# Performance work log

Hardware: AMD Instinct MI355X
Metric: run time of the kernel (lower is better)

The kernel has to match this reference:

```python
import jax, jax.numpy as jnp
import numpy as np

N_NODES = 100000
N_EDGES = 1600000
D_FEAT = 128


def sage_conv(x, src, dst, Wl, Wr, b, n_nodes):
    # gather source features, mean-aggregate at destination (PyG SAGEConv, aggr='mean')
    msgs = x[src]                                            # [E, d]
    agg_sum = jax.ops.segment_sum(msgs, dst, num_segments=n_nodes)
    cnt = jax.ops.segment_sum(jnp.ones((src.shape[0],), dtype=x.dtype), dst,
                              num_segments=n_nodes)
    mean = agg_sum / jnp.maximum(cnt, 1.0)[:, None]
    return mean @ Wl + x @ Wr + b


def setup_inputs() -> dict:
    key = jax.random.key(0)
    ks = jax.random.split(key, 9)
    def w(k, shape):
        fan_in = shape[0]
        return jax.random.normal(k, shape, dtype=jnp.float32) / np.sqrt(fan_in)
    x = jax.random.normal(ks[0], (N_NODES, D_FEAT), dtype=jnp.float32)
    edge_index = jax.random.randint(ks[1], (2, N_EDGES), 0, N_NODES, dtype=jnp.int64)
    return {
        "x": x,
        "edge_index": edge_index,
        "W1l": w(ks[2], (D_FEAT, 64)), "W1r": w(ks[3], (D_FEAT, 64)), "b1": jnp.zeros((64,), jnp.float32),
        "W2l": w(ks[4], (64, 128)),    "W2r": w(ks[5], (64, 128)),    "b2": jnp.zeros((128,), jnp.float32),
        "W3l": w(ks[6], (128, 64)),    "W3r": w(ks[7], (128, 64)),    "b3": jnp.zeros((64,), jnp.float32),
        "Wlin": w(ks[8], (64, 10)),    "blin": jnp.zeros((10,), jnp.float32),
    }


def reference(x, edge_index, W1l, W1r, b1, W2l, W2r, b2, W3l, W3r, b3, Wlin, blin):
    n = x.shape[0]
    src, dst = edge_index[0], edge_index[1]
    # dropout omitted (evaluated in inference / identity form)
    h = jnp.tanh(sage_conv(x, src, dst, W1l, W1r, b1, n))
    h = jnp.tanh(sage_conv(h, src, dst, W2l, W2r, b2, n))
    h = jnp.tanh(sage_conv(h, src, dst, W3l, W3r, b3, n))
    return h @ Wlin + blin
```

## Files before the change

kernel.cpp:

```cpp
#include <hip/hip_runtime.h>

#define THREADS 256
#define NB 256
#define NB_SHIFT 8
#define TILE_E 4096
#define EPT 16
#define BMAXPAD 512
#define WT_LD 136

typedef unsigned short ushort_t;
typedef __attribute__((ext_vector_type(8))) short bf16x8;
typedef __attribute__((ext_vector_type(4))) float f32x4;

__device__ __forceinline__ unsigned short f2bf(float f) {
    unsigned u = __float_as_uint(f);
    u += 0x7fff + ((u >> 16) & 1);
    return (unsigned short)(u >> 16);
}
__device__ __forceinline__ float bf2f(unsigned short s) {
    return __uint_as_float((unsigned)s << 16);
}
__device__ __forceinline__ float4 bf4_to_f4(ushort4 u) {
    return make_float4(bf2f(u.x), bf2f(u.y), bf2f(u.z), bf2f(u.w));
}
__device__ __forceinline__ ushort4 f4_to_bf4(float4 v) {
    ushort4 o;
    o.x = f2bf(v.x); o.y = f2bf(v.y); o.z = f2bf(v.z); o.w = f2bf(v.w);
    return o;
}
__device__ __forceinline__ unsigned pack_bf2(float a, float b) {
    return (unsigned)f2bf(a) | ((unsigned)f2bf(b) << 16);
}
__device__ __forceinline__ void acc_pair(unsigned u, float& lo, float& hi) {
    lo += __uint_as_float(u << 16);
    hi += __uint_as_float(u);
}

__global__ __launch_bounds__(64)
void detect_kernel(const unsigned* __restrict__ ei_words, int* __restrict__ flag) {
    if (threadIdx.x == 0 && blockIdx.x == 0) {
        int allzero = 1;
        for (int i = 0; i < 64; ++i) {
            if (ei_words[2 * i + 1] != 0u) { allzero = 0; break; }
        }
        *flag = allzero;
    }
}

__device__ __forceinline__ void load_edge(const void* ei, int is64, int E, int i,
                                          int& s, int& t) {
    if (is64) {
        const long long* p = (const long long*)ei;
        s = (int)p[i];
        t = (int)p[E + i];
    } else {
        const int* p = (const int*)ei;
        s = p[i];
        t = p[E + i];
    }
}

__global__ __launch_bounds__(256)
void tilesort_kernel(const void* __restrict__ ei, const int* __restrict__ flag,
                     unsigned* __restrict__ tbuf, int* __restrict__ tcnt,
                     int* __restrict__ tstart, int E, int B) {
    __shared__ int hist[BMAXPAD];
    __shared__ int wsum[8];
    const int t   = blockIdx.x;
    const int e0  = t * TILE_E;
    const int is64 = *flag;
    unsigned w[EPT];
    unsigned short bk[EPT];
    for (int i = threadIdx.x; i < BMAXPAD; i += 256) hist[i] = 0;
    __syncthreads();
#pragma unroll
    for (int k = 0; k < EPT; ++k) {
        const int i = e0 + k * 256 + (int)threadIdx.x;
        bk[k] = 0xFFFFu;
        w[k]  = 0u;
        if (i < E) {
            int s, d;
            load_edge(ei, is64, E, i, s, d);
            w[k]  = (unsigned)s | ((unsigned)(d & (NB - 1)) << 17);
            bk[k] = (unsigned short)(d >> NB_SHIFT);
            atomicAdd(&hist[bk[k]], 1);
        }
    }
    __syncthreads();
    const int lane = threadIdx.x & 63;
    const int wid  = threadIdx.x >> 6;
    const int v0 = hist[2 * threadIdx.x];
    const int v1 = hist[2 * threadIdx.x + 1];
    const int sum = v0 + v1;
    int incl = sum;
#pragma unroll
    for (int off = 1; off < 64; off <<= 1) {
        int tt = __shfl_up(incl, off, 64);
        if (lane >= off) incl += tt;
    }
    if (lane == 63) wsum[wid] = incl;
    __syncthreads();
    int woff = 0;
    for (int ww = 0; ww < wid; ++ww) woff += wsum[ww];
    const int excl = woff + incl - sum;
    hist[2 * threadIdx.x]     = excl;
    hist[2 * threadIdx.x + 1] = excl + v0;
    const int b0 = 2 * threadIdx.x, b1 = 2 * threadIdx.x + 1;
    if (b0 < B) { tcnt[(size_t)t * B + b0] = v0; tstart[(size_t)t * B + b0] = excl; }
    if (b1 < B) { tcnt[(size_t)t * B + b1] = v1; tstart[(size_t)t * B + b1] = excl + v0; }
    __syncthreads();
#pragma unroll
    for (int k = 0; k < EPT; ++k) {
        if (bk[k] != 0xFFFFu) {
            const int pos = atomicAdd(&hist[bk[k]], 1);
            tbuf[(size_t)t * TILE_E + pos] = w[k];
        }
    }
}

__global__ __launch_bounds__(256)
void transpose2_kernel(const int* __restrict__ tcnt, const int* __restrict__ tstart,
                       int* __restrict__ tcntT, int* __restrict__ tstartT,
                       int T, int B) {
    __shared__ int ta[32][33];
    __shared__ int tb[32][33];
    const int bx = blockIdx.x;
    const int by = blockIdx.y;
    const int tx = threadIdx.x & 31;
    const int ty = threadIdx.x >> 5;
#pragma unroll
    for (int r = 0; r < 4; ++r) {
        const int trow = by * 32 + ty * 4 + r;
        const int bcol = bx * 32 + tx;
        if (trow < T && bcol < B) {
            ta[ty * 4 + r][tx] = tcnt[(size_t)trow * B + bcol];
            tb[ty * 4 + r][tx] = tstart[(size_t)trow * B + bcol];
        }
    }
    __syncthreads();
#pragma unroll
    for (int r = 0; r < 4; ++r) {
        const int brow = bx * 32 + ty * 4 + r;
        const int tcol = by * 32 + tx;
        if (brow < B && tcol < T) {
            tcntT[(size_t)brow * T + tcol]   = ta[tx][ty * 4 + r];
            tstartT[(size_t)brow * T + tcol] = tb[tx][ty * 4 + r];
        }
    }
}

__global__ __launch_bounds__(256)
void scan_partial_kernel(const int* __restrict__ cnt, int* __restrict__ bsum, int n) {
    const int base = blockIdx.x * 1024;
    int v = 0;
    for (int i = threadIdx.x; i < 1024; i += 256) {
        const int idx = base + i;
        v += (idx < n) ? cnt[idx] : 0;
    }
#pragma unroll
    for (int off = 32; off > 0; off >>= 1) v += __shfl_down(v, off, 64);
    __shared__ int ws[4];
    if ((threadIdx.x & 63) == 0) ws[threadIdx.x >> 6] = v;
    __syncthreads();
    if (threadIdx.x == 0) bsum[blockIdx.x] = ws[0] + ws[1] + ws[2] + ws[3];
}

__global__ __launch_bounds__(64)
void scan_bsum_kernel(int* __restrict__ bsum, int* __restrict__ total, int nb) {
    if (threadIdx.x == 0) {
        int run = 0;
        for (int i = 0; i < nb; ++i) { int t = bsum[i]; bsum[i] = run; run += t; }
        *total = run;
    }
}

__global__ __launch_bounds__(256)
void scan_final_kernel(const int* __restrict__ cnt, const int* __restrict__ bsum,
                       int* __restrict__ outp, int n) {
    const int base = blockIdx.x * 1024 + threadIdx.x * 4;
    int a0 = 0, a1 = 0, a2 = 0, a3 = 0;
    if (base + 0 < n) a0 = cnt[base + 0];
    if (base + 1 < n) a1 = cnt[base + 1];
    if (base + 2 < n) a2 = cnt[base + 2];
    if (base + 3 < n) a3 = cnt[base + 3];
    const int mysum = a0 + a1 + a2 + a3;
    const int lane = threadIdx.x & 63;
    const int wid  = threadIdx.x >> 6;
    int incl = mysum;
#pragma unroll
    for (int off = 1; off < 64; off <<= 1) {
        int t = __shfl_up(incl, off, 64);
        if (lane >= off) incl += t;
    }
    __shared__ int ws[4];
    if (lane == 63) ws[wid] = incl;
    __syncthreads();
    int woff = 0;
    for (int w = 0; w < wid; ++w) woff += ws[w];
    int pre = bsum[blockIdx.x] + woff + (incl - mysum);
    if (base + 0 < n) outp[base + 0] = pre; pre += a0;
    if (base + 1 < n) outp[base + 1] = pre; pre += a1;
    if (base + 2 < n) outp[base + 2] = pre; pre += a2;
    if (base + 3 < n) outp[base + 3] = pre;
}

__global__ __launch_bounds__(256)
void finesort_kernel(const unsigned* __restrict__ tbuf, const int* __restrict__ tcntT,
                     const int* __restrict__ tstartT, const int* __restrict__ hbase,
                     int* __restrict__ rowptr, int* __restrict__ esrc,
                     int n, int E, int T, int B) {
    __shared__ int hist[NB];
    __shared__ int wsum[4];
    const int b  = blockIdx.x;
    const int e0 = hbase[(size_t)b * T];
    hist[threadIdx.x] = 0;
    __syncthreads();
    for (int t = threadIdx.x; t < T; t += 256) {
        const int c  = tcntT[(size_t)b * T + t];
        const int ls = tstartT[(size_t)b * T + t];
        const unsigned* __restrict__ src = tbuf + (size_t)t * TILE_E + ls;
        for (int k = 0; k < c; ++k) atomicAdd(&hist[src[k] >> 17], 1);
    }
    __syncthreads();
    const int lane = threadIdx.x & 63;
    const int wid  = threadIdx.x >> 6;
    const int v = hist[threadIdx.x];
    int incl = v;
#pragma unroll
    for (int off = 1; off < 64; off <<= 1) {
        int tt = __shfl_up(incl, off, 64);
        if (lane >= off) incl += tt;
    }
    if (lane == 63) wsum[wid] = incl;
    __syncthreads();
    int woff = 0;
    for (int w = 0; w < wid; ++w) woff += wsum[w];
    const int excl = woff + incl - v;
    hist[threadIdx.x] = e0 + excl;
    const int node = b * NB + (int)threadIdx.x;
    if (node < n) rowptr[node] = e0 + excl;
    if (b == 0 && threadIdx.x == 0) rowptr[n] = E;
    __syncthreads();
    for (int t = threadIdx.x; t < T; t += 256) {
        const int c  = tcntT[(size_t)b * T + t];
        const int ls = tstartT[(size_t)b * T + t];
        const unsigned* __restrict__ src = tbuf + (size_t)t * TILE_E + ls;
        for (int k = 0; k < c; ++k) {
            const unsigned wv = src[k];
            const int pos = atomicAdd(&hist[wv >> 17], 1);
            esrc[pos] = (int)((wv & 0x1FFFFu) << 8);
        }
    }
}

__global__ __launch_bounds__(256)
void pack_dual_kernel(const float* __restrict__ Wl, const float* __restrict__ Wr,
                      ushort_t* __restrict__ WT) {
    int i = blockIdx.x * 256 + threadIdx.x;
    if (i >= 128 * 128) return;
    int k = i >> 7, c = i & 127;
    float v = (c < 64) ? Wl[k * 64 + c] : Wr[k * 64 + (c - 64)];
    WT[c * WT_LD + k] = f2bf(v);
}
__global__ __launch_bounds__(256)
void pack_stack_kernel(const float* __restrict__ Wl, const float* __restrict__ Wr,
                       ushort_t* __restrict__ WT) {
    int i = blockIdx.x * 256 + threadIdx.x;
    if (i >= 128 * 128) return;
    int k = i >> 7, c = i & 127;
    float v = (k < 64) ? Wl[k * 128 + c] : Wr[(k - 64) * 128 + c];
    WT[c * WT_LD + k] = f2bf(v);
}

template <bool A_FP32, bool TANH_BIAS>
__global__ __launch_bounds__(256)
void mfma_gemm_kernel(const void* __restrict__ Av, const ushort_t* __restrict__ WT,
                      const float* __restrict__ bias, ushort_t* __restrict__ C, int n) {
    __shared__ ushort_t sW[128 * WT_LD];
    {
        const uint4* gsrc = (const uint4*)WT;
        uint4* ldst = (uint4*)sW;
        for (int i = threadIdx.x; i < 128 * WT_LD * 2 / 16; i += 256) ldst[i] = gsrc[i];
    }
    __syncthreads();
    const int lane = threadIdx.x & 63;
    const int wave = threadIdx.x >> 6;
    const int kg   = lane >> 4;
    const int row0 = blockIdx.x * 64 + wave * 16;
    const int rA   = min(row0 + (lane & 15), n - 1);

    bf16x8 a[4];
    if (A_FP32) {
        const float* A = (const float*)Av;
#pragma unroll
        for (int t = 0; t < 4; ++t) {
            const float4 lo = *(const float4*)(A + (size_t)rA * 128 + t * 32 + kg * 8);
            const float4 hi = *(const float4*)(A + (size_t)rA * 128 + t * 32 + kg * 8 + 4);
            const ushort4 u0 = f4_to_bf4(lo), u1 = f4_to_bf4(hi);
            bf16x8 av;
            av[0] = (short)u0.x; av[1] = (short)u0.y; av[2] = (short)u0.z; av[3] = (short)u0.w;
            av[4] = (short)u1.x; av[5] = (short)u1.y; av[6] = (short)u1.z; av[7] = (short)u1.w;
            a[t] = av;
        }
    } else {
        const ushort_t* A = (const ushort_t*)Av;
#pragma unroll
        for (int t = 0; t < 4; ++t)
            a[t] = *(const bf16x8*)(A + (size_t)rA * 128 + t * 32 + kg * 8);
    }

    f32x4 acc[8];
#pragma unroll
    for (int ct = 0; ct < 8; ++ct) acc[ct] = (f32x4)(0.f);

#pragma unroll
    for (int ct = 0; ct < 8; ++ct) {
        const int c0 = ct * 16 + (lane & 15);
#pragma unroll
        for (int t = 0; t < 4; ++t) {
            const bf16x8 b = *(const bf16x8*)(sW + (size_t)c0 * WT_LD + t * 32 + kg * 8);
            acc[ct] = __builtin_amdgcn_mfma_f32_16x16x32_bf16(b, a[t], acc[ct], 0, 0, 0);
        }
    }

    const int r = row0 + (lane & 15);
    if (r < n) {
        ushort_t* crow = C + (size_t)r * 128 + kg * 4;
#pragma unroll
        for (int ct = 0; ct < 8; ++ct) {
            float v0 = acc[ct][0], v1 = acc[ct][1], v2 = acc[ct][2], v3 = acc[ct][3];
            if (TANH_BIAS) {
                const float4 bv = *(const float4*)(bias + ct * 16 + kg * 4);
                v0 = tanhf(v0 + bv.x); v1 = tanhf(v1 + bv.y);
                v2 = tanhf(v2 + bv.z); v3 = tanhf(v3 + bv.w);
            }
            uint2 pk;
            pk.x = pack_bf2(v0, v1);
            pk.y = pack_bf2(v2, v3);
            *(uint2*)(crow + ct * 16) = pk;
        }
    }
}

template <int OUTMODE>
__global__ __launch_bounds__(THREADS)
void gather_fuse_kernel(const int* __restrict__ rowptr, const int* __restrict__ esrc,
                        const ushort_t* __restrict__ pq, const float* __restrict__ bias,
                        ushort_t* __restrict__ hout, int n) {
    constexpr int CH  = 16;
    constexpr int NPB = THREADS / CH;
    const int node = blockIdx.x * NPB + (int)(threadIdx.x / CH);
    const int c    = threadIdx.x & (CH - 1);
    if (node >= n) return;
    const int begin = rowptr[node];
    const int end   = rowptr[node + 1];
    const char* __restrict__ base = (const char*)pq + 8 * c;
    float ax = 0.f, ay = 0.f, az = 0.f, aw = 0.f;
    int e = begin;
    for (; e + 4 <= end; e += 4) {
        const int o0 = esrc[e + 0], o1 = esrc[e + 1], o2 = esrc[e + 2], o3 = esrc[e + 3];
        const uint2 d0 = *(const uint2*)(base + o0);
        const uint2 d1 = *(const uint2*)(base + o1);
        const uint2 d2 = *(const uint2*)(base + o2);
        const uint2 d3 = *(const uint2*)(base + o3);
        acc_pair(d0.x, ax, ay); acc_pair(d0.y, az, aw);
        acc_pair(d1.x, ax, ay); acc_pair(d1.y, az, aw);
        acc_pair(d2.x, ax, ay); acc_pair(d2.y, az, aw);
        acc_pair(d3.x, ax, ay); acc_pair(d3.y, az, aw);
    }
    for (; e < end; ++e) {
        const uint2 d = *(const uint2*)(base + esrc[e]);
        acc_pair(d.x, ax, ay); acc_pair(d.y, az, aw);
    }
    const float inv = 1.0f / fmaxf((float)(end - begin), 1.0f);
    const float4 qv = bf4_to_f4(*(const ushort4*)(pq + (size_t)node * 128 + 64 + 4 * c));
    const float4 bv = *(const float4*)(bias + 4 * c);
    float4 o;
    o.x = tanhf(ax * inv + qv.x + bv.x);
    o.y = tanhf(ay * inv + qv.y + bv.y);
    o.z = tanhf(az * inv + qv.z + bv.z);
    o.w = tanhf(aw * inv + qv.w + bv.w);
    if (OUTMODE == 0) {
        *(ushort4*)(hout + (size_t)node * 128 + 64 + 4 * c) = f4_to_bf4(o);
    } else {
        *(ushort4*)(hout + (size_t)node * 64 + 4 * c) = f4_to_bf4(o);
    }
}

__global__ __launch_bounds__(THREADS)
void gather_mean_kernel(const int* __restrict__ rowptr, const int* __restrict__ esrc,
                        ushort_t* __restrict__ ah, int n) {
    constexpr int CH  = 16;
    constexpr int NPB = THREADS / CH;
    const int node = blockIdx.x * NPB + (int)(threadIdx.x / CH);
    const int c    = threadIdx.x & (CH - 1);
    if (node >= n) return;
    const int begin = rowptr[node];
    const int end   = rowptr[node + 1];
    const char* __restrict__ base = (const char*)ah + 128 + 8 * c;
    float ax = 0.f, ay = 0.f, az = 0.f, aw = 0.f;
    int e = begin;
    for (; e + 4 <= end; e += 4) {
        const int o0 = esrc[e + 0], o1 = esrc[e + 1], o2 = esrc[e + 2], o3 = esrc[e + 3];
        const uint2 d0 = *(const uint2*)(base + o0);
        const uint2 d1 = *(const uint2*)(base + o1);
        const uint2 d2 = *(const uint2*)(base + o2);
        const uint2 d3 = *(const uint2*)(base + o3);
        acc_pair(d0.x, ax, ay); acc_pair(d0.y, az, aw);
        acc_pair(d1.x, ax, ay); acc_pair(d1.y, az, aw);
        acc_pair(d2.x, ax, ay); acc_pair(d2.y, az, aw);
        acc_pair(d3.x, ax, ay); acc_pair(d3.y, az, aw);
    }
    for (; e < end; ++e) {
        const uint2 d = *(const uint2*)(base + esrc[e]);
        acc_pair(d.x, ax, ay); acc_pair(d.y, az, aw);
    }
    const float inv = 1.0f / fmaxf((float)(end - begin), 1.0f);
    ushort4 o = f4_to_bf4(make_float4(ax * inv, ay * inv, az * inv, aw * inv));
    *(ushort4*)(ah + (size_t)node * 128 + 4 * c) = o;
}

__global__ __launch_bounds__(THREADS)
void head_kernel(const ushort_t* __restrict__ h, const float* __restrict__ W,
                 const float* __restrict__ bias, float* __restrict__ out, int n) {
    __shared__ float sW[64 * 10];
    __shared__ float sb[10];
    for (int i = threadIdx.x; i < 640; i += THREADS) sW[i] = W[i];
    if (threadIdx.x < 10) sb[threadIdx.x] = bias[threadIdx.x];
    __syncthreads();
    int idx = blockIdx.x * THREADS + threadIdx.x;
    if (idx >= n * 10) return;
    int row = idx / 10;
    int col = idx - row * 10;
    const uint4* __restrict__ hr = (const uint4*)(h + (size_t)row * 64);
    float acc = sb[col];
#pragma unroll
    for (int k4 = 0; k4 < 8; ++k4) {
        const uint4 u = hr[k4];
        const float* w = sW + (8 * k4) * 10 + col;
        acc += __uint_as_float(u.x << 16)          * w[0];
        acc += __uint_as_float(u.x & 0xffff0000u)  * w[10];
        acc += __uint_as_float(u.y << 16)          * w[20];
        acc += __uint_as_float(u.y & 0xffff0000u)  * w[30];
        acc += __uint_as_float(u.z << 16)          * w[40];
        acc += __uint_as_float(u.z & 0xffff0000u)  * w[50];
        acc += __uint_as_float(u.w << 16)          * w[60];
        acc += __uint_as_float(u.w & 0xffff0000u)  * w[70];
    }
    out[idx] = acc;
}

extern "C" void kernel_launch(void* const* d_in, const int* in_sizes, int n_in,
                              void* d_out, int out_size, void* d_ws, size_t ws_size,
                              hipStream_t stream) {
    const float* x    = (const float*)d_in[0];
    const void*  ei   = d_in[1];
    const float* W1l  = (const float*)d_in[2];
    const float* W1r  = (const float*)d_in[3];
    const float* b1   = (const float*)d_in[4];
    const float* W2l  = (const float*)d_in[5];
    const float* W2r  = (const float*)d_in[6];
    const float* b2   = (const float*)d_in[7];
    const float* W3l  = (const float*)d_in[8];
    const float* W3r  = (const float*)d_in[9];
    const float* b3   = (const float*)d_in[10];
    const float* Wlin = (const float*)d_in[11];
    const float* blin = (const float*)d_in[12];
    float* out = (float*)d_out;

    const int n = in_sizes[0] / 128;
    const int E = in_sizes[1] / 2;
    const int B = (n + NB - 1) / NB;
    const int T = (E + TILE_E - 1) / TILE_E;
    const int Ctot = B * T;

    char* ws = (char*)d_ws;
    size_t off = 0;
    auto carve = [&](size_t bytes) {
        void* p = ws + off;
        off += (bytes + 255) & ~(size_t)255;
        return p;
    };
    int*      flag    = (int*)     carve(256);
    int*      bsum    = (int*)     carve(4096);
    unsigned* tbuf    = (unsigned*)carve((size_t)T * TILE_E * 4);
    int*      tcnt    = (int*)     carve((size_t)Ctot * 4);
    int*      tstart  = (int*)     carve((size_t)Ctot * 4);
    int*      tcntT   = (int*)     carve((size_t)Ctot * 4);
    int*      tstartT = (int*)     carve((size_t)Ctot * 4);
    int*      hbase   = (int*)     carve((size_t)(Ctot + 1) * 4);
    int*      rowptr  = (int*)     carve((size_t)(n + 1) * 4);
    int*      esrc    = (int*)     carve((size_t)E * 4);
    ushort_t* WT1     = (ushort_t*)carve((size_t)128 * WT_LD * 2);
    ushort_t* WT2     = (ushort_t*)carve((size_t)128 * WT_LD * 2);
    ushort_t* WT3     = (ushort_t*)carve((size_t)128 * WT_LD * 2);
    ushort_t* pq      = (ushort_t*)carve((size_t)n * 128 * 2);
    ushort_t* ah      = (ushort_t*)carve((size_t)n * 128 * 2);
    ushort_t* h2      = (ushort_t*)carve((size_t)n * 128 * 2);
    ushort_t* h3      = (ushort_t*)carve((size_t)n * 64 * 2);
    (void)ws_size;

    const int cscan   = (Ctot + 1023) / 1024;
    const int gblocks = (n + 63) / 64;

    pack_dual_kernel <<<64, 256, 0, stream>>>(W1l, W1r, WT1);
    pack_stack_kernel<<<64, 256, 0, stream>>>(W2l, W2r, WT2);
    pack_dual_kernel <<<64, 256, 0, stream>>>(W3l, W3r, WT3);

    detect_kernel<<<1, 64, 0, stream>>>((const unsigned*)ei, flag);
    tilesort_kernel<<<T, 256, 0, stream>>>(ei, flag, tbuf, tcnt, tstart, E, B);
    {
        dim3 tg((B + 31) / 32, (T + 31) / 32);
        transpose2_kernel<<<tg, 256, 0, stream>>>(tcnt, tstart, tcntT, tstartT, T, B);
    }
    scan_partial_kernel<<<cscan, 256, 0, stream>>>(tcntT, bsum, Ctot);
    scan_bsum_kernel<<<1, 64, 0, stream>>>(bsum, hbase + Ctot, cscan);
    scan_final_kernel<<<cscan, 256, 0, stream>>>(tcntT, bsum, hbase, Ctot);
    finesort_kernel<<<B, 256, 0, stream>>>(tbuf, tcntT, tstartT, hbase,
                                           rowptr, esrc, n, E, T, B);

    mfma_gemm_kernel<true, false><<<gblocks, 256, 0, stream>>>(x, WT1, nullptr, pq, n);
    gather_fuse_kernel<0><<<(n + 15) / 16, THREADS, 0, stream>>>(
        rowptr, esrc, pq, b1, ah, n);

    gather_mean_kernel<<<(n + 15) / 16, THREADS, 0, stream>>>(rowptr, esrc, ah, n);
    mfma_gemm_kernel<false, true><<<gblocks, 256, 0, stream>>>(ah, WT2, b2, h2, n);

    mfma_gemm_kernel<false, false><<<gblocks, 256, 0, stream>>>(h2, WT3, nullptr, pq, n);
    gather_fuse_kernel<1><<<(n + 15) / 16, THREADS, 0, stream>>>(
        rowptr, esrc, pq, b3, h3, n);

    head_kernel<<<(n * 10 + THREADS - 1) / THREADS, THREADS, 0, stream>>>(
        h3, Wlin, blin, out, n);
}
```

Before: 256.7 us.

## Shrink sort tiles, widen sort blocks, parallelize block-sum scan, unroll gathers deeper

Edge tiles for the bucket sort shrink from 4096 to 1024 edges, and the tile-sort and fine-sort kernels run with 512 threads. This gives many more tile blocks to spread across the GPU. Because this multiplies the per-tile/per-bucket count matrix, the single-thread serial block-sum scan is replaced by a 1024-thread wave-shuffle scan, and its buffer is enlarged. The two neighbour-gather kernels are also unrolled to issue 8 independent row loads before accumulating, to raise memory-level parallelism. The trade-off is larger count/offset arrays and more transpose and scan work, plus many more nearly empty tile segments that the fine sort must walk per bucket.

```diff
diff --git a/kernel.cpp b/kernel.cpp
--- a/kernel.cpp
+++ b/kernel.cpp
@@ -3,8 +3,8 @@
 #define THREADS 256
 #define NB 256
 #define NB_SHIFT 8
-#define TILE_E 4096
-#define EPT 16
+#define TILE_E 1024
+#define EPT 2
 #define BMAXPAD 512
 #define WT_LD 136
 
@@ -60,7 +60,7 @@
     }
 }
 
-__global__ __launch_bounds__(256)
+__global__ __launch_bounds__(512)
 void tilesort_kernel(const void* __restrict__ ei, const int* __restrict__ flag,
                      unsigned* __restrict__ tbuf, int* __restrict__ tcnt,
                      int* __restrict__ tstart, int E, int B) {
@@ -71,11 +71,11 @@
     const int is64 = *flag;
     unsigned w[EPT];
     unsigned short bk[EPT];
-    for (int i = threadIdx.x; i < BMAXPAD; i += 256) hist[i] = 0;
+    hist[threadIdx.x] = 0;
     __syncthreads();
 #pragma unroll
     for (int k = 0; k < EPT; ++k) {
-        const int i = e0 + k * 256 + (int)threadIdx.x;
+        const int i = e0 + k * 512 + (int)threadIdx.x;
         bk[k] = 0xFFFFu;
         w[k]  = 0u;
         if (i < E) {
@@ -89,10 +89,8 @@
     __syncthreads();
     const int lane = threadIdx.x & 63;
     const int wid  = threadIdx.x >> 6;
-    const int v0 = hist[2 * threadIdx.x];
-    const int v1 = hist[2 * threadIdx.x + 1];
-    const int sum = v0 + v1;
-    int incl = sum;
+    const int v = hist[threadIdx.x];
+    int incl = v;
 #pragma unroll
     for (int off = 1; off < 64; off <<= 1) {
         int tt = __shfl_up(incl, off, 64);
@@ -102,12 +100,10 @@
     __syncthreads();
     int woff = 0;
     for (int ww = 0; ww < wid; ++ww) woff += wsum[ww];
-    const int excl = woff + incl - sum;
-    hist[2 * threadIdx.x]     = excl;
-    hist[2 * threadIdx.x + 1] = excl + v0;
-    const int b0 = 2 * threadIdx.x, b1 = 2 * threadIdx.x + 1;
-    if (b0 < B) { tcnt[(size_t)t * B + b0] = v0; tstart[(size_t)t * B + b0] = excl; }
-    if (b1 < B) { tcnt[(size_t)t * B + b1] = v1; tstart[(size_t)t * B + b1] = excl + v0; }
+    const int excl = woff + incl - v;
+    hist[threadIdx.x] = excl;
+    const int b = threadIdx.x;
+    if (b < B) { tcnt[(size_t)t * B + b] = v; tstart[(size_t)t * B + b] = excl; }
     __syncthreads();
 #pragma unroll
     for (int k = 0; k < EPT; ++k) {
@@ -165,13 +161,40 @@
     if (threadIdx.x == 0) bsum[blockIdx.x] = ws[0] + ws[1] + ws[2] + ws[3];
 }
 
-__global__ __launch_bounds__(64)
+__global__ __launch_bounds__(1024)
 void scan_bsum_kernel(int* __restrict__ bsum, int* __restrict__ total, int nb) {
-    if (threadIdx.x == 0) {
-        int run = 0;
-        for (int i = 0; i < nb; ++i) { int t = bsum[i]; bsum[i] = run; run += t; }
-        *total = run;
-    }
+    __shared__ int wsum[16];
+    const int lane = threadIdx.x & 63;
+    const int wid  = threadIdx.x >> 6;
+    int run = 0;
+    for (int base = 0; base < nb; base += 1024) {
+        const int i = base + (int)threadIdx.x;
+        const int v = (i < nb) ? bsum[i] : 0;
+        int incl = v;
+#pragma unroll
+        for (int off = 1; off < 64; off <<= 1) {
+            int t = __shfl_up(incl, off, 64);
+            if (lane >= off) incl += t;
+        }
+        if (lane == 63) wsum[wid] = incl;
+        __syncthreads();
+        if (wid == 0) {
+            int wv = (lane < 16) ? wsum[lane] : 0;
+#pragma unroll
+            for (int off = 1; off < 16; off <<= 1) {
+                int t = __shfl_up(wv, off, 64);
+                if (lane >= off) wv += t;
+            }
+            if (lane < 16) wsum[lane] = wv;
+        }
+        __syncthreads();
+        const int wbase = (wid > 0) ? wsum[wid - 1] : 0;
+        const int tot   = wsum[15];
+        if (i < nb) bsum[i] = run + wbase + incl - v;
+        run += tot;
+        __syncthreads();
+    }
+    if (threadIdx.x == 0) *total = run;
 }
 
 __global__ __launch_bounds__(256)
@@ -204,7 +227,7 @@
     if (base + 3 < n) outp[base + 3] = pre;
 }
 
-__global__ __launch_bounds__(256)
+__global__ __launch_bounds__(512)
 void finesort_kernel(const unsigned* __restrict__ tbuf, const int* __restrict__ tcntT,
                      const int* __restrict__ tstartT, const int* __restrict__ hbase,
                      int* __restrict__ rowptr, int* __restrict__ esrc,
@@ -213,35 +236,48 @@
     __shared__ int wsum[4];
     const int b  = blockIdx.x;
     const int e0 = hbase[(size_t)b * T];
-    hist[threadIdx.x] = 0;
-    __syncthreads();
-    for (int t = threadIdx.x; t < T; t += 256) {
+    if (threadIdx.x < NB) hist[threadIdx.x] = 0;
+    __syncthreads();
+    for (int t = threadIdx.x; t < T; t += 512) {
         const int c  = tcntT[(size_t)b * T + t];
         const int ls = tstartT[(size_t)b * T + t];
         const unsigned* __restrict__ src = tbuf + (size_t)t * TILE_E + ls;
         for (int k = 0; k < c; ++k) atomicAdd(&hist[src[k] >> 17], 1);
     }
     __syncthreads();
-    const int lane = threadIdx.x & 63;
-    const int wid  = threadIdx.x >> 6;
-    const int v = hist[threadIdx.x];
-    int incl = v;
-#pragma unroll
-    for (int off = 1; off < 64; off <<= 1) {
-        int tt = __shfl_up(incl, off, 64);
-        if (lane >= off) incl += tt;
-    }
-    if (lane == 63) wsum[wid] = incl;
-    __syncthreads();
-    int woff = 0;
-    for (int w = 0; w < wid; ++w) woff += wsum[w];
-    const int excl = woff + incl - v;
-    hist[threadIdx.x] = e0 + excl;
-    const int node = b * NB + (int)threadIdx.x;
-    if (node < n) rowptr[node] = e0 + excl;
+    if (threadIdx.x < NB) {
+        const int lane = threadIdx.x & 63;
+        const int wid  = threadIdx.x >> 6;
+        const int v = hist[threadIdx.x];
+        int incl = v;
+#pragma unroll
+        for (int off = 1; off < 64; off <<= 1) {
+            int tt = __shfl_up(incl, off, 64);
+            if (lane >= off) incl += tt;
+        }
+        if (lane == 63) wsum[wid] = incl;
+    }
+    __syncthreads();
+    if (threadIdx.x < NB) {
+        const int wid = threadIdx.x >> 6;
+        const int v   = hist[threadIdx.x];
+        const int lane = threadIdx.x & 63;
+        int incl = v;
+#pragma unroll
+        for (int off = 1; off < 64; off <<= 1) {
+            int tt = __shfl_up(incl, off, 64);
+            if (lane >= off) incl += tt;
+        }
+        int woff = 0;
+        for (int w = 0; w < wid; ++w) woff += wsum[w];
+        const int excl = woff + incl - v;
+        hist[threadIdx.x] = e0 + excl;
+        const int node = b * NB + (int)threadIdx.x;
+        if (node < n) rowptr[node] = e0 + excl;
+    }
     if (b == 0 && threadIdx.x == 0) rowptr[n] = E;
     __syncthreads();
-    for (int t = threadIdx.x; t < T; t += 256) {
+    for (int t = threadIdx.x; t < T; t += 512) {
         const int c  = tcntT[(size_t)b * T + t];
         const int ls = tstartT[(size_t)b * T + t];
         const unsigned* __restrict__ src = tbuf + (size_t)t * TILE_E + ls;
@@ -357,16 +393,20 @@
     const char* __restrict__ base = (const char*)pq + 8 * c;
     float ax = 0.f, ay = 0.f, az = 0.f, aw = 0.f;
     int e = begin;
-    for (; e + 4 <= end; e += 4) {
-        const int o0 = esrc[e + 0], o1 = esrc[e + 1], o2 = esrc[e + 2], o3 = esrc[e + 3];
-        const uint2 d0 = *(const uint2*)(base + o0);
-        const uint2 d1 = *(const uint2*)(base + o1);
-        const uint2 d2 = *(const uint2*)(base + o2);
-        const uint2 d3 = *(const uint2*)(base + o3);
-        acc_pair(d0.x, ax, ay); acc_pair(d0.y, az, aw);
-        acc_pair(d1.x, ax, ay); acc_pair(d1.y, az, aw);
-        acc_pair(d2.x, ax, ay); acc_pair(d2.y, az, aw);
-        acc_pair(d3.x, ax, ay); acc_pair(d3.y, az, aw);
+    for (; e + 8 <= end; e += 8) {
+        uint2 d[8];
+#pragma unroll
+        for (int j = 0; j < 8; ++j) d[j] = *(const uint2*)(base + esrc[e + j]);
+#pragma unroll
+        for (int j = 0; j < 8; ++j) { acc_pair(d[j].x, ax, ay); acc_pair(d[j].y, az, aw); }
+    }
+    if (e + 4 <= end) {
+        uint2 d[4];
+#pragma unroll
+        for (int j = 0; j < 4; ++j) d[j] = *(const uint2*)(base + esrc[e + j]);
+#pragma unroll
+        for (int j = 0; j < 4; ++j) { acc_pair(d[j].x, ax, ay); acc_pair(d[j].y, az, aw); }
+        e += 4;
     }
     for (; e < end; ++e) {
         const uint2 d = *(const uint2*)(base + esrc[e]);
@@ -400,16 +440,20 @@
     const char* __restrict__ base = (const char*)ah + 128 + 8 * c;
     float ax = 0.f, ay = 0.f, az = 0.f, aw = 0.f;
     int e = begin;
-    for (; e + 4 <= end; e += 4) {
-        const int o0 = esrc[e + 0], o1 = esrc[e + 1], o2 = esrc[e + 2], o3 = esrc[e + 3];
-        const uint2 d0 = *(const uint2*)(base + o0);
-        const uint2 d1 = *(const uint2*)(base + o1);
-        const uint2 d2 = *(const uint2*)(base + o2);
-        const uint2 d3 = *(const uint2*)(base + o3);
-        acc_pair(d0.x, ax, ay); acc_pair(d0.y, az, aw);
-        acc_pair(d1.x, ax, ay); acc_pair(d1.y, az, aw);
-        acc_pair(d2.x, ax, ay); acc_pair(d2.y, az, aw);
-        acc_pair(d3.x, ax, ay); acc_pair(d3.y, az, aw);
+    for (; e + 8 <= end; e += 8) {
+        uint2 d[8];
+#pragma unroll
+        for (int j = 0; j < 8; ++j) d[j] = *(const uint2*)(base + esrc[e + j]);
+#pragma unroll
+        for (int j = 0; j < 8; ++j) { acc_pair(d[j].x, ax, ay); acc_pair(d[j].y, az, aw); }
+    }
+    if (e + 4 <= end) {
+        uint2 d[4];
+#pragma unroll
+        for (int j = 0; j < 4; ++j) d[j] = *(const uint2*)(base + esrc[e + j]);
+#pragma unroll
+        for (int j = 0; j < 4; ++j) { acc_pair(d[j].x, ax, ay); acc_pair(d[j].y, az, aw); }
+        e += 4;
     }
     for (; e < end; ++e) {
         const uint2 d = *(const uint2*)(base + esrc[e]);
@@ -482,7 +526,7 @@
         return p;
     };
     int*      flag    = (int*)     carve(256);
-    int*      bsum    = (int*)     carve(4096);
+    int*      bsum    = (int*)     carve(8192);
     unsigned* tbuf    = (unsigned*)carve((size_t)T * TILE_E * 4);
     int*      tcnt    = (int*)     carve((size_t)Ctot * 4);
     int*      tstart  = (int*)     carve((size_t)Ctot * 4);
@@ -508,15 +552,15 @@
     pack_dual_kernel <<<64, 256, 0, stream>>>(W3l, W3r, WT3);
 
     detect_kernel<<<1, 64, 0, stream>>>((const unsigned*)ei, flag);
-    tilesort_kernel<<<T, 256, 0, stream>>>(ei, flag, tbuf, tcnt, tstart, E, B);
+    tilesort_kernel<<<T, 512, 0, stream>>>(ei, flag, tbuf, tcnt, tstart, E, B);
     {
         dim3 tg((B + 31) / 32, (T + 31) / 32);
         transpose2_kernel<<<tg, 256, 0, stream>>>(tcnt, tstart, tcntT, tstartT, T, B);
     }
     scan_partial_kernel<<<cscan, 256, 0, stream>>>(tcntT, bsum, Ctot);
-    scan_bsum_kernel<<<1, 64, 0, stream>>>(bsum, hbase + Ctot, cscan);
+    scan_bsum_kernel<<<1, 1024, 0, stream>>>(bsum, hbase + Ctot, cscan);
     scan_final_kernel<<<cscan, 256, 0, stream>>>(tcntT, bsum, hbase, Ctot);
-    finesort_kernel<<<B, 256, 0, stream>>>(tbuf, tcntT, tstartT, hbase,
+    finesort_kernel<<<B, 512, 0, stream>>>(tbuf, tcntT, tstartT, hbase,
                                            rowptr, esrc, n, E, T, B);
 
     mfma_gemm_kernel<true, false><<<gblocks, 256, 0, stream>>>(x, WT1, nullptr, pq, n);
```

Result: faster. 245.8 us (-4.2%).
